# Performance work log

Hardware: AMD Instinct MI355X
Metric: run time of the kernel (lower is better)

The kernel has to match this reference:

```python
import jax, jax.numpy as jnp
import numpy as np

B_, N, C = 4096, 49, 384
H = 12
HD = C // H
NW = 64
SCALE = HD ** -0.5


def setup_inputs() -> dict:
    key = jax.random.key(0)
    k_x, k_m, k_w1, k_b1, k_w2, k_b2 = jax.random.split(key, 6)
    x = jax.random.normal(k_x, (B_, N, C), dtype=jnp.float32)
    # shifted-window style additive mask: 0 = allowed, -100 = blocked
    mask = jnp.where(jax.random.uniform(k_m, (NW, N, N)) < 0.5, 0.0, -100.0).astype(jnp.float32)
    w_qkv = jax.random.normal(k_w1, (3 * C, C), dtype=jnp.float32) * (C ** -0.5)
    b_qkv = jax.random.normal(k_b1, (3 * C,), dtype=jnp.float32) * 0.02
    w_proj = jax.random.normal(k_w2, (C, C), dtype=jnp.float32) * (C ** -0.5)
    b_proj = jax.random.normal(k_b2, (C,), dtype=jnp.float32) * 0.02
    return {"x": x, "mask": mask, "w_qkv": w_qkv, "b_qkv": b_qkv,
            "w_proj": w_proj, "b_proj": b_proj}


def reference(x, mask, w_qkv, b_qkv, w_proj, b_proj):
    # qkv projection: (B_, N, 3C)
    qkv = x @ w_qkv.T + b_qkv
    qkv = qkv.reshape(B_, N, 3, H, HD).transpose(2, 0, 3, 1, 4)  # (3, B_, H, N, HD)
    q, k, v = qkv[0], qkv[1], qkv[2]
    q = q * SCALE
    attn = jnp.einsum('bhnd,bhmd->bhnm', q, k)  # (B_, H, N, N)
    # additive shifted-window mask, per-window pattern broadcast over batch & heads
    attn = attn.reshape(B_ // NW, NW, H, N, N) + mask[None, :, None]
    attn = attn.reshape(B_, H, N, N)
    attn = jax.nn.softmax(attn, axis=-1)
    out = jnp.einsum('bhnm,bhmd->bhnd', attn, v)  # (B_, H, N, HD)
    out = out.transpose(0, 2, 1, 3).reshape(B_, N, C)
    return out @ w_proj.T + b_proj
```

## Files before the change

kernel.cpp:

```cpp
#include <hip/hip_runtime.h>
#include <cstdio>
#include <cstdint>


typedef __attribute__((ext_vector_type(8))) short bfrag8;
typedef __attribute__((ext_vector_type(4))) float facc4;
typedef __attribute__((ext_vector_type(16))) float facc16;

#define SCALE_Q 0.17677669529663687f
#define PLANE 6422528ull

__device__ __forceinline__ unsigned short f2bf(float f) {
  unsigned int x = __float_as_uint(f);
  x += 0x7fffu + ((x >> 16) & 1u);
  return (unsigned short)(x >> 16);
}

__device__ __forceinline__ void gload_lds16(const void* g, void* l) {
  __builtin_amdgcn_global_load_lds(
      (const __attribute__((address_space(1))) unsigned int*)g,
      (__attribute__((address_space(3))) unsigned int*)l,
      16, 0, 0);
}

__global__ void __launch_bounds__(256) mask_bits_kernel(
    const float* __restrict__ mask, unsigned long long* __restrict__ bits) {
  const int idx = blockIdx.x * 256 + threadIdx.x;
  const int wdw = idx >> 6, m = idx & 63;
  unsigned long long bm = 0ull;
  if (m < 49) {
    const float* mp = mask + (size_t)wdw * 2401 + (size_t)m * 49;
    for (int n = 0; n < 49; ++n)
      if (mp[n] > -50.f) bm |= (1ull << n);
  }
  bits[idx] = bm;
}

__global__ void __launch_bounds__(256) wswz32_kernel(const float* __restrict__ w,
                                                     unsigned short* __restrict__ Bf) {
  const int t = blockIdx.x * 256 + threadIdx.x;
  const int fid = t >> 6, lc = t & 63;
  const int cg = fid / 24, ksl = fid - cg * 24;
  const int col = cg * 32 + (lc & 31);
  const int k = ksl * 16 + (lc >> 5) * 8;
  const float* src = w + (size_t)col * 384 + k;
  unsigned short* dst = Bf + ((size_t)fid << 9) + (lc << 3);
#pragma unroll
  for (int j = 0; j < 8; ++j) dst[j] = f2bf(src[j]);
}

#define LB32(dst, ks_)                                                         \
  {                                                                            \
    _Pragma("unroll") for (int ni = 0; ni < 3; ++ni)                           \
        dst[ni] = *(const bfrag8*)(                                            \
            Bf + ((size_t)((cg0 + ni) * 24 + (ks_)) << 9) + (lane << 3));      \
  }

#define MF32(bb, ks_)                                                          \
  {                                                                            \
    const bfrag8 af0 = *(const bfrag8*)(Ab + ((size_t)(ks_) << 10));           \
    const bfrag8 af1 = *(const bfrag8*)(Ab + ((size_t)(24 + (ks_)) << 10));    \
    _Pragma("unroll") for (int ni = 0; ni < 3; ++ni) {                         \
      acc[0][ni] = __builtin_amdgcn_mfma_f32_32x32x16_bf16(af0, bb[ni],        \
                                                           acc[0][ni], 0, 0, 0);\
      acc[1][ni] = __builtin_amdgcn_mfma_f32_32x32x16_bf16(af1, bb[ni],        \
                                                           acc[1][ni], 0, 0, 0);\
    }                                                                          \
  }

template <int NR, int MODE, int SWZ>
__global__ void __launch_bounds__(512, 1) gemm_32(
    const float* __restrict__ Af32, const unsigned short* __restrict__ Abf,
    const unsigned short* __restrict__ Bf, const float* __restrict__ bias,
    unsigned short* __restrict__ qkv, float* __restrict__ f_out) {
  __shared__ __align__(16) unsigned short Alds[128 * 384];

  int bid = blockIdx.x;
  bid = (bid & 7) * SWZ + (bid >> 3);
  const int tid = threadIdx.x;
  const int lane = tid & 63, w = tid >> 6;
  const int wr = w >> 2, wc = w & 3;
  const int l31 = lane & 31, l5 = lane >> 5;
  const size_t a_row0 = (size_t)bid * 128;

  if (MODE == 0) {
    const int arow = tid >> 2, seg = tid & 3;
    const float* asrc = Af32 + (a_row0 + arow) * 384 + seg * 96;
    const int rg = arow >> 5, lifr = arow & 31;
#pragma unroll
    for (int j = 0; j < 24; ++j) {
      const int k0 = seg * 96 + j * 4;
      const float4 v = *(const float4*)(asrc + j * 4);
      ushort4 h4;
      h4.x = f2bf(v.x); h4.y = f2bf(v.y); h4.z = f2bf(v.z); h4.w = f2bf(v.w);
      const int fid = rg * 24 + (k0 >> 4);
      const int lif = lifr + ((k0 & 15) >> 3) * 32;
      *(ushort4*)((char*)Alds + ((size_t)fid << 10) + (lif << 4) +
                  ((k0 & 7) << 1)) = h4;
    }
  } else {
#pragma unroll
    for (int j = 0; j < 12; ++j) {
      const int fid = w + j * 8;
      const int rg = fid / 24, ksl = fid - rg * 24;
      const int row = rg * 32 + l31;
      const int k = ksl * 16 + l5 * 8;
      gload_lds16(Abf + (a_row0 + row) * 384 + k,
                  (char*)Alds + ((w << 10) + (j << 13)));
    }
  }
  __syncthreads();

  const char* Ab = (const char*)Alds + ((size_t)(wr * 48) << 10) + (lane << 4);

  for (int rnd = 0; rnd < NR; ++rnd) {
    const int cg0 = (rnd * 4 + wc) * 3;
    facc16 acc[2][3];
#pragma unroll
    for (int mi = 0; mi < 2; ++mi)
#pragma unroll
      for (int ni = 0; ni < 3; ++ni)
#pragma unroll
        for (int r = 0; r < 16; ++r) acc[mi][ni][r] = 0.f;

    bfrag8 bA[3], bB[3], bC[3];
    LB32(bA, 0);
    LB32(bB, 1);
    LB32(bC, 2);
#pragma unroll 1
    for (int ks = 0; ks < 24; ks += 3) {
      MF32(bA, ks);
      if (ks + 3 < 24) LB32(bA, ks + 3);
      MF32(bB, ks + 1);
      if (ks + 4 < 24) LB32(bB, ks + 4);
      MF32(bC, ks + 2);
      if (ks + 5 < 24) LB32(bC, ks + 5);
    }

    if (MODE == 0) {
#pragma unroll
      for (int ni = 0; ni < 3; ++ni) {
        const int j0 = (cg0 + ni) * 32;
        const int t = j0 / 384;
        const int rj = j0 - t * 384;
        const int h = rj >> 5;
        unsigned short* pl = qkv + (size_t)(t * 12 + h) * PLANE + l31;
        const float bvv = bias[j0 + l31];
        const float sc = (t == 0) ? SCALE_Q : 1.0f;
#pragma unroll
        for (int mi = 0; mi < 2; ++mi)
#pragma unroll
          for (int r = 0; r < 16; ++r) {
            const size_t m = a_row0 + wr * 64 + mi * 32 +
                             (r & 3) + 8 * (r >> 2) + 4 * l5;
            pl[m * 32] = f2bf((acc[mi][ni][r] + bvv) * sc);
          }
      }
    } else {
#pragma unroll
      for (int ni = 0; ni < 3; ++ni) {
        const int col = (cg0 + ni) * 32 + l31;
        const float bvv = bias[col];
#pragma unroll
        for (int mi = 0; mi < 2; ++mi)
#pragma unroll
          for (int r = 0; r < 16; ++r) {
            const size_t m = a_row0 + wr * 64 + mi * 32 +
                             (r & 3) + 8 * (r >> 2) + 4 * l5;
            f_out[m * 384 + col] = acc[mi][ni][r] + bvv;
          }
      }
    }
  }
}

__global__ void __launch_bounds__(64) attn_kernel(
    const unsigned short* __restrict__ QKV,
    const unsigned long long* __restrict__ mbits,
    unsigned short* __restrict__ Og) {
  __shared__ unsigned short Vt[32 * 64];
  __shared__ unsigned short Ps[64 * 64];

  const int bid = blockIdx.x;
  const int b = bid / 12, h = bid - b * 12;
  const int lane = threadIdx.x;
  const int l15 = lane & 15, l4 = lane >> 4;

  const bfrag8 z8 = {0, 0, 0, 0, 0, 0, 0, 0};
  const facc4 fz = {0.f, 0.f, 0.f, 0.f};

  const size_t wb = (size_t)b * 49 * 32;
  const unsigned short* Qp = QKV + (size_t)h * PLANE + wb;
  const unsigned short* Kp = QKV + (size_t)(12 + h) * PLANE + wb;
  const unsigned short* Vp = QKV + (size_t)(24 + h) * PLANE + wb;

#pragma unroll
  for (int i = 0; i < 4; ++i)
    *(bfrag8*)((char*)Vt + (lane + i * 64) * 16) = z8;

#pragma unroll
  for (int i = 0; i < 4; ++i) {
    const int c = lane + i * 64;
    if (c < 196) {
      const bfrag8 vv = *(const bfrag8*)(Vp + c * 8);
      const int n = c >> 2, cc = c & 3;
      const int d0 = cc * 8;
#pragma unroll
      for (int jj = 0; jj < 8; ++jj) {
        const int d = d0 + jj;
        *(unsigned short*)((char*)Vt + (((d << 7) + (n << 1)) ^ ((d & 7) << 4))) =
            (unsigned short)vv[jj];
      }
    }
  }
  __syncthreads();

  facc4 s[4][4];
  {
    bfrag8 qa[4], kf[4];
#pragma unroll
    for (int mi = 0; mi < 4; ++mi)
      qa[mi] = *(const bfrag8*)((const char*)Qp + (mi * 16 + l15) * 64 + l4 * 16);
#pragma unroll
    for (int ni = 0; ni < 4; ++ni)
      kf[ni] = *(const bfrag8*)((const char*)Kp + (ni * 16 + l15) * 64 + l4 * 16);
#pragma unroll
    for (int mi = 0; mi < 4; ++mi)
#pragma unroll
      for (int ni = 0; ni < 4; ++ni)
        s[mi][ni] = __builtin_amdgcn_mfma_f32_16x16x32_bf16(qa[mi], kf[ni], fz, 0, 0, 0);
  }

  const unsigned long long* mb = mbits + (size_t)(b & 63) * 64;
  float rinv[4][4];
#pragma unroll
  for (int mi = 0; mi < 4; ++mi)
#pragma unroll
    for (int r = 0; r < 4; ++r) {
      const int m = mi * 16 + l4 * 4 + r;
      const unsigned long long mw = mb[m];
      float mx = -1e30f;
      int ok[4];
#pragma unroll
      for (int ni = 0; ni < 4; ++ni) {
        const int n = ni * 16 + l15;
        ok[ni] = (int)((mw >> n) & 1ull);
        const float v = ok[ni] ? s[mi][ni][r] : -1e30f;
        mx = fmaxf(mx, v);
      }
      mx = fmaxf(mx, __shfl_xor(mx, 1));
      mx = fmaxf(mx, __shfl_xor(mx, 2));
      mx = fmaxf(mx, __shfl_xor(mx, 4));
      mx = fmaxf(mx, __shfl_xor(mx, 8));
      float sum = 0.f;
#pragma unroll
      for (int ni = 0; ni < 4; ++ni) {
        const float p = ok[ni] ? __expf(s[mi][ni][r] - mx) : 0.f;
        s[mi][ni][r] = p;
        sum += p;
      }
      sum += __shfl_xor(sum, 1);
      sum += __shfl_xor(sum, 2);
      sum += __shfl_xor(sum, 4);
      sum += __shfl_xor(sum, 8);
      rinv[mi][r] = 1.0f / sum;
#pragma unroll
      for (int ni = 0; ni < 4; ++ni) {
        const int n = ni * 16 + l15;
        *(unsigned short*)((char*)Ps + (((m << 7) + (n << 1)) ^ ((m & 7) << 4))) =
            f2bf(s[mi][ni][r]);
      }
    }
  __syncthreads();

  facc4 o[4][2];
#pragma unroll
  for (int mi = 0; mi < 4; ++mi)
#pragma unroll
    for (int di = 0; di < 2; ++di) o[mi][di] = fz;
#pragma unroll
  for (int kk = 0; kk < 2; ++kk) {
    bfrag8 pa[4], vb[2];
#pragma unroll
    for (int mi = 0; mi < 4; ++mi) {
      const int row = mi * 16 + l15;
      pa[mi] = *(const bfrag8*)((const char*)Ps +
                                (((row << 7) + kk * 64 + (l4 << 4)) ^ ((row & 7) << 4)));
    }
#pragma unroll
    for (int di = 0; di < 2; ++di) {
      const int row = di * 16 + l15;
      vb[di] = *(const bfrag8*)((const char*)Vt +
                                (((row << 7) + kk * 64 + (l4 << 4)) ^ ((row & 7) << 4)));
    }
#pragma unroll
    for (int mi = 0; mi < 4; ++mi)
#pragma unroll
      for (int di = 0; di < 2; ++di)
        o[mi][di] = __builtin_amdgcn_mfma_f32_16x16x32_bf16(pa[mi], vb[di], o[mi][di], 0, 0, 0);
  }

  unsigned short* op = Og + (size_t)b * 18816 + h * 32;
#pragma unroll
  for (int mi = 0; mi < 4; ++mi)
#pragma unroll
    for (int r = 0; r < 4; ++r) {
      const int m = mi * 16 + l4 * 4 + r;
      if (m < 49) {
        const float rs = rinv[mi][r];
#pragma unroll
        for (int di = 0; di < 2; ++di)
          op[(size_t)m * 384 + di * 16 + l15] = f2bf(o[mi][di][r] * rs);
      }
    }
}

extern "C" void kernel_launch(void* const* d_in, const int* in_sizes, int n_in,
                              void* d_out, int out_size, void* d_ws, size_t ws_size,
                              hipStream_t stream) {
  const float* x      = (const float*)d_in[0];
  const float* mask   = (const float*)d_in[1];
  const float* w_qkv  = (const float*)d_in[2];
  const float* b_qkv  = (const float*)d_in[3];
  const float* w_proj = (const float*)d_in[4];
  const float* b_proj = (const float*)d_in[5];
  float* out = (float*)d_out;

  const size_t E = 77070336ull;
  unsigned short* wsu   = (unsigned short*)d_ws;
  unsigned short* qkvp  = wsu;
  unsigned short* o_ws  = wsu + 3 * E;
  unsigned short* Bfq   = wsu + 4 * E;
  unsigned short* Bfp   = Bfq + 442368ull;
  unsigned long long* mb = (unsigned long long*)(Bfp + 147456ull);
  const size_t need = (4 * E + 442368ull + 147456ull) * 2ull + 4096ull * 8ull;
  if (ws_size < need) {
    fprintf(stderr, "[WindowAttention] ws too small: need=%zu have=%zu\n",
            (size_t)need, ws_size);
    return;
  }

  wswz32_kernel<<<216, 256, 0, stream>>>(w_qkv, Bfq);
  wswz32_kernel<<<72, 256, 0, stream>>>(w_proj, Bfp);
  mask_bits_kernel<<<16, 256, 0, stream>>>(mask, mb);

  gemm_32<3, 0, 196><<<1568, 512, 0, stream>>>(x, nullptr, Bfq, b_qkv,
                                               qkvp, nullptr);

  attn_kernel<<<49152, 64, 0, stream>>>(qkvp, mb, o_ws);

  gemm_32<1, 1, 196><<<1568, 512, 0, stream>>>(nullptr, o_ws, Bfp, b_proj,
                                               nullptr, out);
}
```

Before: 669.8 us.

## Write V transposed from QKV GEMM epilogue and merge prep kernels

The QKV GEMM epilogue now writes the V head planes pre-transposed (head dim by token, padded to 64 tokens per window). The attention kernel can then load V^T fragments straight from global memory instead of zero-filling and transposing V through LDS with a barrier. The three small preprocessing kernels are folded into one launch. The cost is scattered, poorly coalesced 2-byte stores in the GEMM epilogue for the V columns, and the padded token columns 49..63 of V^T are never written, so they rely on whatever the workspace already holds being multiplied by zero probabilities.

```diff
diff --git a/kernel.cpp b/kernel.cpp
--- a/kernel.cpp
+++ b/kernel.cpp
@@ -9,6 +9,8 @@
 
 #define SCALE_Q 0.17677669529663687f
 #define PLANE 6422528ull
+#define VOFF 154140672ull
+#define VH 8388608ull
 
 __device__ __forceinline__ unsigned short f2bf(float f) {
   unsigned int x = __float_as_uint(f);
@@ -23,30 +25,35 @@
       16, 0, 0);
 }
 
-__global__ void __launch_bounds__(256) mask_bits_kernel(
-    const float* __restrict__ mask, unsigned long long* __restrict__ bits) {
-  const int idx = blockIdx.x * 256 + threadIdx.x;
-  const int wdw = idx >> 6, m = idx & 63;
-  unsigned long long bm = 0ull;
-  if (m < 49) {
-    const float* mp = mask + (size_t)wdw * 2401 + (size_t)m * 49;
-    for (int n = 0; n < 49; ++n)
-      if (mp[n] > -50.f) bm |= (1ull << n);
-  }
-  bits[idx] = bm;
-}
-
-__global__ void __launch_bounds__(256) wswz32_kernel(const float* __restrict__ w,
-                                                     unsigned short* __restrict__ Bf) {
-  const int t = blockIdx.x * 256 + threadIdx.x;
-  const int fid = t >> 6, lc = t & 63;
-  const int cg = fid / 24, ksl = fid - cg * 24;
-  const int col = cg * 32 + (lc & 31);
-  const int k = ksl * 16 + (lc >> 5) * 8;
-  const float* src = w + (size_t)col * 384 + k;
-  unsigned short* dst = Bf + ((size_t)fid << 9) + (lc << 3);
-#pragma unroll
-  for (int j = 0; j < 8; ++j) dst[j] = f2bf(src[j]);
+__global__ void __launch_bounds__(256) prep_kernel(
+    const float* __restrict__ wq, const float* __restrict__ wp,
+    const float* __restrict__ mask,
+    unsigned short* __restrict__ Bfq, unsigned short* __restrict__ Bfp,
+    unsigned long long* __restrict__ bits) {
+  const int blk = blockIdx.x;
+  if (blk < 288) {
+    const float* w = (blk < 216) ? wq : wp;
+    unsigned short* Bf = (blk < 216) ? Bfq : Bfp;
+    const int t = ((blk < 216) ? blk : blk - 216) * 256 + threadIdx.x;
+    const int fid = t >> 6, lc = t & 63;
+    const int cg = fid / 24, ksl = fid - cg * 24;
+    const int col = cg * 32 + (lc & 31);
+    const int k = ksl * 16 + (lc >> 5) * 8;
+    const float* src = w + (size_t)col * 384 + k;
+    unsigned short* dst = Bf + ((size_t)fid << 9) + (lc << 3);
+#pragma unroll
+    for (int j = 0; j < 8; ++j) dst[j] = f2bf(src[j]);
+  } else {
+    const int idx = (blk - 288) * 256 + threadIdx.x;
+    const int wdw = idx >> 6, m = idx & 63;
+    unsigned long long bm = 0ull;
+    if (m < 49) {
+      const float* mp = mask + (size_t)wdw * 2401 + (size_t)m * 49;
+      for (int n = 0; n < 49; ++n)
+        if (mp[n] > -50.f) bm |= (1ull << n);
+    }
+    bits[idx] = bm;
+  }
 }
 
 #define LB32(dst, ks_)                                                         \
@@ -144,17 +151,31 @@
         const int t = j0 / 384;
         const int rj = j0 - t * 384;
         const int h = rj >> 5;
-        unsigned short* pl = qkv + (size_t)(t * 12 + h) * PLANE + l31;
         const float bvv = bias[j0 + l31];
-        const float sc = (t == 0) ? SCALE_Q : 1.0f;
-#pragma unroll
-        for (int mi = 0; mi < 2; ++mi)
-#pragma unroll
-          for (int r = 0; r < 16; ++r) {
-            const size_t m = a_row0 + wr * 64 + mi * 32 +
-                             (r & 3) + 8 * (r >> 2) + 4 * l5;
-            pl[m * 32] = f2bf((acc[mi][ni][r] + bvv) * sc);
-          }
+        if (t < 2) {
+          unsigned short* pl = qkv + (size_t)(t * 12 + h) * PLANE + l31;
+          const float sc = (t == 0) ? SCALE_Q : 1.0f;
+#pragma unroll
+          for (int mi = 0; mi < 2; ++mi)
+#pragma unroll
+            for (int r = 0; r < 16; ++r) {
+              const size_t m = a_row0 + wr * 64 + mi * 32 +
+                               (r & 3) + 8 * (r >> 2) + 4 * l5;
+              pl[m * 32] = f2bf((acc[mi][ni][r] + bvv) * sc);
+            }
+        } else {
+          unsigned short* vp = qkv + VOFF + (size_t)h * VH + (size_t)l31 * 64;
+#pragma unroll
+          for (int mi = 0; mi < 2; ++mi)
+#pragma unroll
+            for (int r = 0; r < 16; ++r) {
+              const unsigned int m = (unsigned int)(a_row0 + wr * 64 + mi * 32 +
+                                                    (r & 3) + 8 * (r >> 2) + 4 * l5);
+              const unsigned int bq = m / 49u;
+              const unsigned int nn = m - bq * 49u;
+              vp[(size_t)bq * 2048 + nn] = f2bf(acc[mi][ni][r] + bvv);
+            }
+        }
       }
     } else {
 #pragma unroll
@@ -178,7 +199,6 @@
     const unsigned short* __restrict__ QKV,
     const unsigned long long* __restrict__ mbits,
     unsigned short* __restrict__ Og) {
-  __shared__ unsigned short Vt[32 * 64];
   __shared__ unsigned short Ps[64 * 64];
 
   const int bid = blockIdx.x;
@@ -186,34 +206,12 @@
   const int lane = threadIdx.x;
   const int l15 = lane & 15, l4 = lane >> 4;
 
-  const bfrag8 z8 = {0, 0, 0, 0, 0, 0, 0, 0};
   const facc4 fz = {0.f, 0.f, 0.f, 0.f};
 
   const size_t wb = (size_t)b * 49 * 32;
   const unsigned short* Qp = QKV + (size_t)h * PLANE + wb;
   const unsigned short* Kp = QKV + (size_t)(12 + h) * PLANE + wb;
-  const unsigned short* Vp = QKV + (size_t)(24 + h) * PLANE + wb;
-
-#pragma unroll
-  for (int i = 0; i < 4; ++i)
-    *(bfrag8*)((char*)Vt + (lane + i * 64) * 16) = z8;
-
-#pragma unroll
-  for (int i = 0; i < 4; ++i) {
-    const int c = lane + i * 64;
-    if (c < 196) {
-      const bfrag8 vv = *(const bfrag8*)(Vp + c * 8);
-      const int n = c >> 2, cc = c & 3;
-      const int d0 = cc * 8;
-#pragma unroll
-      for (int jj = 0; jj < 8; ++jj) {
-        const int d = d0 + jj;
-        *(unsigned short*)((char*)Vt + (((d << 7) + (n << 1)) ^ ((d & 7) << 4))) =
-            (unsigned short)vv[jj];
-      }
-    }
-  }
-  __syncthreads();
+  const unsigned short* Vtg = QKV + VOFF + (size_t)h * VH + (size_t)b * 2048;
 
   facc4 s[4][4];
   {
@@ -288,11 +286,9 @@
                                 (((row << 7) + kk * 64 + (l4 << 4)) ^ ((row & 7) << 4)));
     }
 #pragma unroll
-    for (int di = 0; di < 2; ++di) {
-      const int row = di * 16 + l15;
-      vb[di] = *(const bfrag8*)((const char*)Vt +
-                                (((row << 7) + kk * 64 + (l4 << 4)) ^ ((row & 7) << 4)));
-    }
+    for (int di = 0; di < 2; ++di)
+      vb[di] = *(const bfrag8*)((const char*)Vtg +
+                                (di * 16 + l15) * 128 + kk * 64 + l4 * 16);
 #pragma unroll
     for (int mi = 0; mi < 4; ++mi)
 #pragma unroll
@@ -327,22 +323,21 @@
   float* out = (float*)d_out;
 
   const size_t E = 77070336ull;
+  const size_t QKVE = 254803968ull;
   unsigned short* wsu   = (unsigned short*)d_ws;
   unsigned short* qkvp  = wsu;
-  unsigned short* o_ws  = wsu + 3 * E;
-  unsigned short* Bfq   = wsu + 4 * E;
+  unsigned short* o_ws  = wsu + QKVE;
+  unsigned short* Bfq   = o_ws + E;
   unsigned short* Bfp   = Bfq + 442368ull;
   unsigned long long* mb = (unsigned long long*)(Bfp + 147456ull);
-  const size_t need = (4 * E + 442368ull + 147456ull) * 2ull + 4096ull * 8ull;
+  const size_t need = (QKVE + E + 442368ull + 147456ull) * 2ull + 4096ull * 8ull;
   if (ws_size < need) {
     fprintf(stderr, "[WindowAttention] ws too small: need=%zu have=%zu\n",
             (size_t)need, ws_size);
     return;
   }
 
-  wswz32_kernel<<<216, 256, 0, stream>>>(w_qkv, Bfq);
-  wswz32_kernel<<<72, 256, 0, stream>>>(w_proj, Bfp);
-  mask_bits_kernel<<<16, 256, 0, stream>>>(mask, mb);
+  prep_kernel<<<304, 256, 0, stream>>>(w_qkv, w_proj, mask, Bfq, Bfp, mb);
 
   gemm_32<3, 0, 196><<<1568, 512, 0, stream>>>(x, nullptr, Bfq, b_qkv,
                                                qkvp, nullptr);
```

After: 844.3 us. 1.26x slower.
